# Optimization experiments

Measured on AMD Instinct MI355X. Metric: run time of the kernel, lower is better.

Reference implementation:

```python
import jax, jax.numpy as jnp
import numpy as np

B, H, W, ENC = 64, 14, 14, 2048
A, E, D, V, T = 512, 512, 512, 10000, 21


def setup_inputs() -> dict:
    key = jax.random.key(0)
    ks = jax.random.split(key, 24)
    f = lambda k, shape, s: (jax.random.normal(k, shape, jnp.float32) * s)
    inp = {
        'encoder_out': f(ks[0], (B, H, W, ENC), 1.0),
        'encoded_captions': jax.random.randint(ks[1], (B, T), 0, V),
        'caption_lengths': jax.random.randint(ks[2], (B,), 0, T + 1),
        'emb': jax.random.uniform(ks[3], (V, E), jnp.float32, -0.1, 0.1),
        'enc_att_W': f(ks[4], (ENC, A), 0.02), 'enc_att_b': jnp.zeros((A,), jnp.float32),
        'dec_att_W': f(ks[5], (D, A), 0.04), 'dec_att_b': jnp.zeros((A,), jnp.float32),
        'full_att_W': f(ks[6], (A, 1), 0.04), 'full_att_b': jnp.zeros((1,), jnp.float32),
        'init_h_W': f(ks[7], (ENC, D), 0.02), 'init_h_b': jnp.zeros((D,), jnp.float32),
        'init_c_W': f(ks[8], (ENC, D), 0.02), 'init_c_b': jnp.zeros((D,), jnp.float32),
        'f_beta_W': f(ks[9], (D, ENC), 0.04), 'f_beta_b': jnp.zeros((ENC,), jnp.float32),
        'W_ih': f(ks[10], (4 * D, E + ENC), 0.02), 'b_ih': jnp.zeros((4 * D,), jnp.float32),
        'W_hh': f(ks[11], (4 * D, D), 0.04), 'b_hh': jnp.zeros((4 * D,), jnp.float32),
        'fc_W': jax.random.uniform(ks[12], (D, V), jnp.float32, -0.1, 0.1),
        'fc_b': jnp.zeros((V,), jnp.float32),
    }
    return inp


def reference(encoder_out, encoded_captions, caption_lengths, emb,
              enc_att_W, enc_att_b, dec_att_W, dec_att_b, full_att_W, full_att_b,
              init_h_W, init_h_b, init_c_W, init_c_b, f_beta_W, f_beta_b,
              W_ih, b_ih, W_hh, b_hh, fc_W, fc_b):
    b = encoder_out.shape[0]
    enc = encoder_out.reshape(b, -1, encoder_out.shape[-1])  # (B, P, ENC)
    cl = jnp.clip(caption_lengths.reshape(-1), 1, None)
    sort_ind = jnp.argsort(-cl)  # descending by length
    cl = cl[sort_ind]
    enc = enc[sort_ind]
    caps = encoded_captions[sort_ind]
    dec_len = cl - 1  # (B,)

    embs = emb[caps]  # (B, T, E)
    mean_enc = enc.mean(axis=1)
    h0 = jnp.tanh(mean_enc @ init_h_W + init_h_b)
    c0 = jnp.tanh(mean_enc @ init_c_W + init_c_b)

    att1 = enc @ enc_att_W + enc_att_b  # (B, P, A), loop-invariant
    Tdec = caps.shape[1] - 1
    embs_t = jnp.swapaxes(embs[:, :Tdec], 0, 1)  # (Tdec, B, E)

    def step(carry, xs):
        h, c = carry
        t, x_emb = xs
        active = (t < dec_len)[:, None]  # (B,1)
        att2 = h @ dec_att_W + dec_att_b  # (B, A)
        e = jnp.squeeze(jax.nn.relu(att1 + att2[:, None, :]) @ full_att_W, -1) + full_att_b[0]  # (B,P)
        alpha = jax.nn.softmax(e + 1e-8, axis=1)
        awe = jnp.einsum('bpe,bp->be', enc, alpha)  # (B, ENC)
        gate = jax.nn.sigmoid(h @ f_beta_W + f_beta_b)
        awe = gate * awe
        x = jnp.concatenate([x_emb, awe], axis=1)  # (B, E+ENC)
        gates = x @ W_ih.T + b_ih + h @ W_hh.T + b_hh  # (B, 4D)
        i, f, g, o = jnp.split(gates, 4, axis=1)
        c_new = jax.nn.sigmoid(f) * c + jax.nn.sigmoid(i) * jnp.tanh(g)
        h_new = jax.nn.sigmoid(o) * jnp.tanh(c_new)
        preds = h_new @ fc_W + fc_b
        h = jnp.where(active, h_new, h)
        c = jnp.where(active, c_new, c)
        preds = jnp.where(active, preds, 0.0)
        alpha = jnp.where(active, alpha, 0.0)
        return (h, c), (preds, alpha)

    (_, _), (preds, alphas) = jax.lax.scan(step, (h0, c0), (jnp.arange(Tdec), embs_t))
    predictions = jnp.swapaxes(preds, 0, 1)  # (B, Tdec, V)
    alphas = jnp.swapaxes(alphas, 0, 1)      # (B, Tdec, P)
    return predictions, caps, dec_len, alphas, sort_ind
```

## Files before the change

kernel.cpp:

```cpp
#include <hip/hip_runtime.h>
#include <hip/hip_cooperative_groups.h>
#include <cstddef>


namespace cg = cooperative_groups;

namespace {

typedef _Float16 f16;
typedef f16 f16x8 __attribute__((ext_vector_type(8)));
typedef f16 f16x4 __attribute__((ext_vector_type(4)));
typedef f16 f16x2 __attribute__((ext_vector_type(2)));
typedef float f32x4 __attribute__((ext_vector_type(4)));

constexpr int NB = 64, NP = 196, NE = 2048, NA = 512, ND = 512, NV = 10000;
constexpr int NT_CAP = 21, NTD = 20;
constexpr int KC = 3072;
constexpr int LDT = 40;
constexpr int LDK = 72;

constexpr size_t OFF_ATT1   = 0;
constexpr size_t OFF_DAW    = 12845056;
constexpr size_t OFF_FBW    = 13369344;
constexpr size_t OFF_EAW    = 15466496;
constexpr size_t OFF_IHW    = 17563648;
constexpr size_t OFF_ICW    = 19660800;
constexpr size_t OFF_FCW    = 15466496;
constexpr size_t OFF_WCAT   = 25755648;
constexpr size_t OFF_MEAN16 = 38338560;
constexpr size_t OFF_H16    = 38600704;
constexpr size_t OFF_HNEW16 = 38666240;
constexpr size_t OFF_C      = 38731776;
constexpr size_t OFF_ATT2   = 38862848;
constexpr size_t OFF_GATE   = 38993920;
constexpr size_t OFF_ALPHA  = 39518208;
constexpr size_t OFF_XCAT   = 39569408;
constexpr size_t OFF_INT    = 39962624;
constexpr size_t OFF_BCAT   = 39970816;
constexpr size_t OFF_ENC16  = 39979008;
constexpr size_t FULL_BYTES = 91359232;
constexpr size_t OFF_HSEQ   = FULL_BYTES;
constexpr size_t FULL2_BYTES = FULL_BYTES + (size_t)NTD * NB * ND * 2;
constexpr size_t OFF_HWHH   = FULL2_BYTES;
constexpr size_t OFF_EMBW   = OFF_HWHH + 524288;
constexpr size_t OFF_EMBS   = OFF_EMBW + 10485760;
constexpr size_t FULL3_BYTES = OFF_EMBS + 1310720;

__device__ __forceinline__ float sigmoidf_(float x) { return 1.0f / (1.0f + expf(-x)); }

__device__ __forceinline__ void stage16(const f16* __restrict__ src, int lda, int k0,
                                        f16* __restrict__ lds, int tid) {
  const int row = tid >> 2, seg = tid & 3;
  *(f16x8*)&lds[row * LDT + seg * 8] =
      *(const f16x8*)&src[(size_t)row * lda + k0 + seg * 8];
}

__device__ __forceinline__ void cvt8(const float* __restrict__ p, f16* __restrict__ dst) {
  const float4 a = *(const float4*)p;
  const float4 b = *(const float4*)(p + 4);
  f16x8 v;
  v[0] = (f16)a.x; v[1] = (f16)a.y; v[2] = (f16)a.z; v[3] = (f16)a.w;
  v[4] = (f16)b.x; v[5] = (f16)b.y; v[6] = (f16)b.z; v[7] = (f16)b.w;
  *(f16x8*)dst = v;
}

__device__ __forceinline__ void wave_gemm64(const f16* __restrict__ A,
                                            const f16* __restrict__ Brow, int K,
                                            int kbeg, int kend,
                                            int col, int quad, f32x4* acc) {
  for (int k0 = kbeg; k0 < kend; k0 += 32) {
    const int kk = k0 + quad * 8;
    const f16x8 b = *(const f16x8*)&Brow[(size_t)col * K + kk];
#pragma unroll
    for (int mt = 0; mt < 4; ++mt) {
      const f16x8 a = *(const f16x8*)&A[(size_t)(mt * 16 + col) * K + kk];
      acc[mt] = __builtin_amdgcn_mfma_f32_16x16x32_f16(a, b, acc[mt], 0, 0, 0);
    }
  }
}

template <int MT>
__device__ __forceinline__ void wave_gemm_s(const f16* __restrict__ A, int lda,
                                            const f16* __restrict__ Brow, int ldb,
                                            int kbeg, int kend,
                                            int col, int quad, f32x4* acc) {
  for (int k0 = kbeg; k0 < kend; k0 += 32) {
    const int kk = k0 + quad * 8;
    const f16x8 b = *(const f16x8*)&Brow[(size_t)col * ldb + kk];
#pragma unroll
    for (int mt = 0; mt < MT; ++mt) {
      const f16x8 a = *(const f16x8*)&A[(size_t)(mt * 16 + col) * lda + kk];
      acc[mt] = __builtin_amdgcn_mfma_f32_16x16x32_f16(a, b, acc[mt], 0, 0, 0);
    }
  }
}

__global__ void k_sort(const int* __restrict__ cap_len, const int* __restrict__ caps,
                       int* __restrict__ perm, int* __restrict__ declen,
                       int* __restrict__ caps_sorted,
                       float* __restrict__ out_caps, float* __restrict__ out_declen,
                       float* __restrict__ out_sortind) {
  __shared__ int cl[NB];
  __shared__ int pr[NB];
  const int i = threadIdx.x;
  int c = cap_len[i];
  if (c < 1) c = 1;
  cl[i] = c;
  __syncthreads();
  int rank = 0;
  for (int j = 0; j < NB; ++j) {
    const int cj = cl[j];
    if (cj > c || (cj == c && j < i)) rank++;
  }
  pr[rank] = i;
  __syncthreads();
  const int src = pr[i];
  perm[i] = src;
  const int dl = cl[src] - 1;
  declen[i] = dl;
  out_declen[i] = (float)dl;
  out_sortind[i] = (float)src;
  for (int j = 0; j < NT_CAP; ++j) {
    const int v = caps[src * NT_CAP + j];
    caps_sorted[i * NT_CAP + j] = v;
    out_caps[i * NT_CAP + j] = (float)v;
  }
}

__global__ __launch_bounds__(256) void k_tconv(const float* __restrict__ src,
                                               f16* __restrict__ dst, int K, int Nsrc) {
  __shared__ float tile[32][33];
  const int n0 = blockIdx.x * 32, k0 = blockIdx.y * 32;
  const int tid = threadIdx.x;
  const int a = tid & 31, q = tid >> 5;
#pragma unroll
  for (int r = 0; r < 4; ++r) {
    const int kl = q * 4 + r;
    tile[a][kl] = (n0 + a < Nsrc) ? src[(size_t)(k0 + kl) * Nsrc + n0 + a] : 0.0f;
  }
  __syncthreads();
#pragma unroll
  for (int r = 0; r < 4; ++r) {
    const int nl = q * 4 + r;
    dst[(size_t)(n0 + nl) * K + k0 + a] = (f16)tile[nl][a];
  }
}

__global__ __launch_bounds__(256) void k_cvt_wcat2(const float* __restrict__ Wih,
                                                   const float* __restrict__ Whh,
                                                   const float* __restrict__ bih,
                                                   const float* __restrict__ bhh,
                                                   f16* __restrict__ Wcat2,
                                                   float* __restrict__ bcat) {
  const int r = blockIdx.x;
  const int d = r >> 2, g = r & 3;
  const int n = g * 512 + d;
  for (int k = threadIdx.x; k < KC; k += 256) {
    const float v = (k < 2560) ? Wih[(size_t)n * 2560 + k] : Whh[(size_t)n * 512 + (k - 2560)];
    Wcat2[(size_t)r * KC + k] = (f16)v;
  }
  if (threadIdx.x == 0) bcat[r] = bih[n] + bhh[n];
}

__global__ __launch_bounds__(256) void k_mean(const float* __restrict__ enc,
                                              const int* __restrict__ perm,
                                              f16* __restrict__ mean16) {
  const int b = blockIdx.y;
  const int c0 = blockIdx.x * 512 + threadIdx.x * 2;
  const float* base = enc + (size_t)perm[b] * NP * NE + c0;
  float a0 = 0.0f, a1 = 0.0f;
  for (int p = 0; p < NP; ++p) {
    const float2 v = *(const float2*)&base[(size_t)p * NE];
    a0 += v.x; a1 += v.y;
  }
  mean16[(size_t)b * NE + c0] = (f16)(a0 * (1.0f / (float)NP));
  mean16[(size_t)b * NE + c0 + 1] = (f16)(a1 * (1.0f / (float)NP));
}

__global__ __launch_bounds__(256) void k_mean16(const f16* __restrict__ enc16,
                                                f16* __restrict__ mean16) {
  const int b = blockIdx.y;
  const int c0 = blockIdx.x * 512 + threadIdx.x * 2;
  const f16* base = enc16 + (size_t)b * NP * NE + c0;
  float a0 = 0.0f, a1 = 0.0f;
  for (int p = 0; p < NP; ++p) {
    const f16x2 v = *(const f16x2*)&base[(size_t)p * NE];
    a0 += (float)v[0]; a1 += (float)v[1];
  }
  mean16[(size_t)b * NE + c0] = (f16)(a0 * (1.0f / (float)NP));
  mean16[(size_t)b * NE + c0 + 1] = (f16)(a1 * (1.0f / (float)NP));
}

__global__ __launch_bounds__(256) void k_enc_cvt(const float* __restrict__ enc,
                                                 const int* __restrict__ perm,
                                                 f16* __restrict__ enc16) {
  const int p = blockIdx.x, b = blockIdx.y;
  const float* src = enc + ((size_t)perm[b] * NP + p) * NE;
  f16* dst = enc16 + ((size_t)b * NP + p) * NE;
  const int i0 = threadIdx.x * 8;
  cvt8(src + i0, dst + i0);
}

__global__ __launch_bounds__(256) void k_embs(const float* __restrict__ emb,
                                              const int* __restrict__ caps_s,
                                              f16* __restrict__ embs16) {
  const int t = blockIdx.x, b = blockIdx.y;
  const int cap = caps_s[b * NT_CAP + t];
  const int i0 = threadIdx.x * 2;
  const float2 v = *(const float2*)(emb + (size_t)cap * 512 + i0);
  f16x2 ev; ev[0] = (f16)v.x; ev[1] = (f16)v.y;
  *(f16x2*)&embs16[((size_t)t * NB + b) * 512 + i0] = ev;
}

__global__ __launch_bounds__(256) void k_embw(const f16* __restrict__ embs16,
                                              const f16* __restrict__ Wcat2,
                                              float* __restrict__ embw) {
  __shared__ __align__(16) f16 lA[256 * LDK];
  __shared__ __align__(16) f16 lB[64 * LDK];
  const int n0 = blockIdx.x * 64, m0 = blockIdx.y * 256;
  const int tid = threadIdx.x, lane = tid & 63, wv = tid >> 6;
  const int col = lane & 15, quad = lane >> 4;
  const f16* gA = embs16 + (size_t)(m0 + tid) * 512;
  const f16* gB = Wcat2 + (size_t)(n0 + (tid >> 2)) * KC + (tid & 3) * 16;
  f16* wA = &lA[tid * LDK];
  f16* wB = &lB[(tid >> 2) * LDK + (tid & 3) * 16];
  f32x4 acc[4][4] = {};
  for (int k0 = 0; k0 < 512; k0 += 64) {
// ... 40 lines not shown
                                                   const float* __restrict__ icb,
                                                   f16* __restrict__ h16,
                                                   float* __restrict__ cst) {
  const int which = blockIdx.y;
  const f16* Wt = which ? icWt : ihWt;
  const float* bias = which ? icb : ihb;
  const int tid = threadIdx.x, lane = tid & 63, wv = tid >> 6;
  const int col = lane & 15, quad = lane >> 4;
  const int nt = blockIdx.x * 4 + wv;
  f32x4 acc[4] = {};
  wave_gemm64(mean16, Wt + (size_t)nt * 16 * NE, NE, 0, NE, col, quad, acc);
  const int n = nt * 16 + col;
#pragma unroll
  for (int mt = 0; mt < 4; ++mt) {
#pragma unroll
    for (int rr = 0; rr < 4; ++rr) {
      const int m = mt * 16 + quad * 4 + rr;
      const float v = tanhf(acc[mt][rr] + bias[n]);
      if (which == 0) h16[(size_t)m * ND + n] = (f16)v;
      else            cst[(size_t)m * ND + n] = v;
    }
  }
}

template <bool E16>
__global__ __launch_bounds__(256) void k_att1_mfma(const float* __restrict__ encf,
                                                   const f16* __restrict__ enc16,
                                                   const int* __restrict__ perm,
                                                   const f16* __restrict__ eaWt,
                                                   const float* __restrict__ eab,
                                                   f16* __restrict__ att1) {
  __shared__ __align__(16) f16 lA[64 * LDT];
  __shared__ __align__(16) f16 lB[128 * LDT];
  __shared__ int rowoff[64];
  const int r0 = blockIdx.y * 64;
  const int n0 = blockIdx.x * 128;
  const int tid = threadIdx.x, lane = tid & 63, wv = tid >> 6;
  const int col = lane & 15, quad = lane >> 4;
  if (!E16) {
    if (tid < 64) {
      const int r = r0 + tid;
      const int b = r / NP, p = r - b * NP;
      rowoff[tid] = (perm[b] * NP + p) * NE;
    }
    __syncthreads();
  }
  f32x4 acc[8] = {};
  for (int k0 = 0; k0 < NE; k0 += 32) {
    if (E16) {
      stage16(enc16 + (size_t)r0 * NE, NE, k0, lA, tid);
    } else {
      const int row = tid >> 2, seg = tid & 3;
      cvt8(encf + (size_t)rowoff[row] + k0 + seg * 8, &lA[row * LDT + seg * 8]);
    }
    {
      const int row0 = tid >> 2, seg = tid & 3;
#pragma unroll
      for (int u = 0; u < 2; ++u) {
        const int row = row0 + 64 * u;
        *(f16x8*)&lB[row * LDT + seg * 8] =
            *(const f16x8*)&eaWt[(size_t)(n0 + row) * NE + k0 + seg * 8];
      }
    }
    __syncthreads();
    const f16x8 a = *(const f16x8*)&lA[(wv * 16 + col) * LDT + quad * 8];
#pragma unroll
    for (int ns = 0; ns < 8; ++ns) {
      const f16x8 b = *(const f16x8*)&lB[(ns * 16 + col) * LDT + quad * 8];
      acc[ns] = __builtin_amdgcn_mfma_f32_16x16x32_f16(a, b, acc[ns], 0, 0, 0);
    }
    __syncthreads();
  }
#pragma unroll
  for (int ns = 0; ns < 8; ++ns) {
    const int n = n0 + ns * 16 + col;
#pragma unroll
    for (int rr = 0; rr < 4; ++rr) {
      const int r = r0 + wv * 16 + quad * 4 + rr;
      att1[(size_t)r * NA + n] = (f16)(acc[ns][rr] + eab[n]);
    }
  }
}

__global__ __launch_bounds__(256) void k_att1_v2(const f16* __restrict__ enc16,
                                                 const f16* __restrict__ eaWt,
                                                 const float* __restrict__ eab,
                                                 f16* __restrict__ att1) {
  __shared__ __align__(16) f16 lA[64 * LDK];
  __shared__ __align__(16) f16 lB[128 * LDK];
  const int r0 = blockIdx.x * 64, n0 = blockIdx.y * 128;
  const int tid = threadIdx.x, lane = tid & 63, wv = tid >> 6;
  const int col = lane & 15, quad = lane >> 4;
  const int wr = wv >> 1, wc = wv & 1;
  const int arow = tid >> 2, aseg = (tid & 3) * 16;
  const int brow = tid >> 1, bseg = (tid & 1) * 32;
  const f16* gA = enc16 + (size_t)(r0 + arow) * NE + aseg;
  const f16* gB = eaWt + (size_t)(n0 + brow) * NE + bseg;
  f16* wA = &lA[arow * LDK + aseg];
  f16* wB = &lB[brow * LDK + bseg];
  f32x4 acc[2][4] = {};
  for (int k0 = 0; k0 < NE; k0 += 64) {
    *(f16x8*)(wA)      = *(const f16x8*)(gA + k0);
    *(f16x8*)(wA + 8)  = *(const f16x8*)(gA + k0 + 8);
    *(f16x8*)(wB)      = *(const f16x8*)(gB + k0);
    *(f16x8*)(wB + 8)  = *(const f16x8*)(gB + k0 + 8);
    *(f16x8*)(wB + 16) = *(const f16x8*)(gB + k0 + 16);
    *(f16x8*)(wB + 24) = *(const f16x8*)(gB + k0 + 24);
    __syncthreads();
#pragma unroll
    for (int kh = 0; kh < 2; ++kh) {
      f16x8 a[2], b[4];
#pragma unroll
      for (int i = 0; i < 2; ++i)
        a[i] = *(const f16x8*)&lA[(wr * 32 + i * 16 + col) * LDK + kh * 32 + quad * 8];
#pragma unroll
      for (int j = 0; j < 4; ++j)
        b[j] = *(const f16x8*)&lB[(wc * 64 + j * 16 + col) * LDK + kh * 32 + quad * 8];
#pragma unroll
      for (int i = 0; i < 2; ++i)
#pragma unroll
        for (int j = 0; j < 4; ++j)
          acc[i][j] = __builtin_amdgcn_mfma_f32_16x16x32_f16(a[i], b[j], acc[i][j], 0, 0, 0);
    }
    __syncthreads();
  }
#pragma unroll
  for (int j = 0; j < 4; ++j) {
    const int n = n0 + wc * 64 + j * 16 + col;
    const float bv = eab[n];
#pragma unroll
    for (int i = 0; i < 2; ++i)
#pragma unroll
      for (int rr = 0; rr < 4; ++rr) {
        const int r = r0 + wr * 32 + i * 16 + quad * 4 + rr;
        att1[(size_t)r * NA + n] = (f16)(acc[i][j][rr] + bv);
      }
  }
}

struct StepParams {
  f16* h16;
  const f16* daWt; const float* dab;
  const f16* fbWt; const float* fbb;
  const f16* Wcat2; const float* bcat;
  const f16* att1; const float* fullW;
  const f16* enc16;
  const float* embw;
  const int* declen;
  float* att2; float* gate; float* hwhh;
  float* alpha; float* out_alphas;
  f16* xcat;
  float* cst;
  f16* hseq;
};

__global__ __launch_bounds__(512, 2) void k_steps(StepParams P) {
  cg::grid_group grid = cg::this_grid();
  __shared__ float S[8192];
  const int tid = threadIdx.x, lane = tid & 63, wv = tid >> 6;
  const int col = lane & 15, quad = lane >> 4;
  const int bid = blockIdx.x, nblk = gridDim.x;

  for (int t = 0; t < NTD; ++t) {
    for (int nt = bid; nt < 288; nt += nblk) {
      const f16* Brow; int ldb;
      if (nt < 32)       { Brow = P.daWt + (size_t)nt * 16 * ND; ldb = ND; }
      else if (nt < 160) { Brow = P.fbWt + (size_t)(nt - 32) * 16 * ND; ldb = ND; }
      else               { Brow = P.Wcat2 + (size_t)(nt - 160) * 16 * KC + 2560; ldb = KC; }
      f32x4 acc[4] = {};
      wave_gemm_s<4>(P.h16, ND, Brow, ldb, wv * 64, wv * 64 + 64, col, quad, acc);
#pragma unroll
      for (int mt = 0; mt < 4; ++mt)
#pragma unroll
        for (int rr = 0; rr < 4; ++rr)
          S[wv * 1024 + (mt * 4 + rr) * 64 + lane] = acc[mt][rr];
      __syncthreads();
#pragma unroll
      for (int j = 0; j < 2; ++j) {
        const int slot = tid * 2 + j;
        float s = S[slot];
#pragma unroll
        for (int w = 1; w < 8; ++w) s += S[w * 1024 + slot];
        const int c2 = slot >> 6, lane_s = slot & 63;
        const int mt = c2 >> 2, rr = c2 & 3;
        const int m = mt * 16 + (lane_s >> 4) * 4 + rr;
        const int nl = lane_s & 15;
        if (nt < 32) {
          const int n = nt * 16 + nl;
          P.att2[(size_t)m * NA + n] = s + P.dab[n];
        } else if (nt < 160) {
          const int n = (nt - 32) * 16 + nl;
          P.gate[(size_t)m * NE + n] = sigmoidf_(s + P.fbb[n]);
        } else {
          const int r = (nt - 160) * 16 + nl;
          P.hwhh[(size_t)m * NE + r] = s;
        }
      }
      __syncthreads();
    }
    __threadfence();
    grid.sync();

    for (int b = bid; b < NB; b += nblk) {
      float a2r[8], fwr[8];
      {
        const float4* A2 = (const float4*)(P.att2 + (size_t)b * NA + lane * 8);
        const float4* FW = (const float4*)(P.fullW + lane * 8);
        const float4 q0 = A2[0], q1 = A2[1], w0 = FW[0], w1 = FW[1];
        a2r[0] = q0.x; a2r[1] = q0.y; a2r[2] = q0.z; a2r[3] = q0.w;
        a2r[4] = q1.x; a2r[5] = q1.y; a2r[6] = q1.z; a2r[7] = q1.w;
        fwr[0] = w0.x; fwr[1] = w0.y; fwr[2] = w0.z; fwr[3] = w0.w;
        fwr[4] = w1.x; fwr[5] = w1.y; fwr[6] = w1.z; fwr[7] = w1.w;
      }
      for (int p = wv; p < NP; p += 8) {
        const f16x8 row = *(const f16x8*)(P.att1 + ((size_t)b * NP + p) * NA + lane * 8);
        float acc = 0.0f;
#pragma unroll
        for (int j = 0; j < 8; ++j) acc += fmaxf((float)row[j] + a2r[j], 0.0f) * fwr[j];
#pragma unroll
        for (int off = 32; off > 0; off >>= 1) acc += __shfl_down(acc, off, 64);
        if (lane == 0) S[p] = acc;
      }
      __syncthreads();
      if (wv == 0) {
        const float v0 = S[lane];
        const float v1 = S[lane + 64];
        const float v2 = S[lane + 128];
        const float v3 = (lane < 4) ? S[192 + lane] : -INFINITY;
        float mx = fmaxf(fmaxf(v0, v1), fmaxf(v2, v3));
#pragma unroll
        for (int off = 32; off > 0; off >>= 1) mx = fmaxf(mx, __shfl_xor(mx, off, 64));
        float s = expf(v0 - mx) + expf(v1 - mx) + expf(v2 - mx) +
                  ((lane < 4) ? expf(v3 - mx) : 0.0f);
#pragma unroll
        for (int off = 32; off > 0; off >>= 1) s += __shfl_xor(s, off, 64);
        if (lane == 0) { S[200] = mx; S[201] = 1.0f / s; }
      }
      __syncthreads();
      if (tid < NP) {
        const float a = expf(S[tid] - S[200]) * S[201];
        P.alpha[(size_t)b * NP + tid] = a;
        const bool act = t < P.declen[b];
        P.out_alphas[((size_t)b * NTD + t) * NP + tid] = act ? a : 0.0f;
      }
      __syncthreads();
    }
    __threadfence();
    grid.sync();

    for (int task = bid; task < 256; task += nblk) {
      const int b = task >> 2, q = task & 3;
      if (tid < NP) S[tid] = P.alpha[(size_t)b * NP + tid];
      __syncthreads();
      const int cl = (tid & 255) * 2, ph = tid >> 8;
      const int c = q * 512 + cl;
      const f16* base = P.enc16 + (size_t)b * NP * NE + c;
      float a0 = 0.0f, a1 = 0.0f;
      const int p0 = ph ? 98 : 0, p1 = ph ? 196 : 98;
      for (int p = p0; p < p1; ++p) {
        const f16x2 v = *(const f16x2*)&base[(size_t)p * NE];
        const float ap = S[p];
        a0 += ap * (float)v[0]; a1 += ap * (float)v[1];
      }
      S[256 + ph * 512 + cl] = a0;
      S[256 + ph * 512 + cl + 1] = a1;
      __syncthreads();
      if (tid < 256) {
        const int c2 = tid * 2;
        const float r0 = S[256 + c2] + S[768 + c2];
        const float r1 = S[256 + c2 + 1] + S[768 + c2 + 1];
        const int cc = q * 512 + c2;
        const float2 g = *(const float2*)&P.gate[(size_t)b * NE + cc];
        f16x2 o; o[0] = (f16)(r0 * g.x); o[1] = (f16)(r1 * g.y);
        *(f16x2*)&P.xcat[(size_t)b * KC + 512 + cc] = o;
      }
      __syncthreads();
    }
    __threadfence();
    grid.sync();

    for (int task = bid; task < 256; task += nblk) {
      const int nt = task >> 1, mh = task & 1;
      f32x4 acc[2] = {};
      wave_gemm_s<2>(P.xcat + (size_t)mh * 32 * KC, KC,
                     P.Wcat2 + (size_t)nt * 16 * KC, KC,
                     512 + wv * 256, 512 + wv * 256 + 256, col, quad, acc);
#pragma unroll
      for (int mt = 0; mt < 2; ++mt)
#pragma unroll
        for (int rr = 0; rr < 4; ++rr)
          S[wv * 512 + (mt * 4 + rr) * 64 + lane] = acc[mt][rr];
      __syncthreads();
      {
        float s = S[tid];
#pragma unroll
        for (int w = 1; w < 8; ++w) s += S[w * 512 + tid];
        S[tid] = s;
      }
      __syncthreads();
      if (tid < 128) {
        const int ml = tid >> 2, dl = tid & 3;
        const int m = mh * 32 + ml;
        const int d = nt * 4 + dl;
        const int mt = ml >> 4, qd = (ml >> 2) & 3, rr = ml & 3;
        float g4[4];
#pragma unroll
        for (int g = 0; g < 4; ++g) {
          const int cv = dl * 4 + g;
          const int r = nt * 16 + cv;
          g4[g] = S[(mt * 4 + rr) * 64 + qd * 16 + cv] + P.bcat[r] +
                  P.hwhh[(size_t)m * NE + r] + P.embw[((size_t)t * NB + m) * NE + r];
        }
        const float iv = sigmoidf_(g4[0]);
        const float fv = sigmoidf_(g4[1]);
        const float gv = tanhf(g4[2]);
        const float ov = sigmoidf_(g4[3]);
        const float cold = P.cst[(size_t)m * ND + d];
        const float cn = fv * cold + iv * gv;
        const float hn = ov * tanhf(cn);
        P.hseq[((size_t)t * NB + m) * ND + d] = (f16)hn;
        if (t < P.declen[m]) {
          P.cst[(size_t)m * ND + d] = cn;
          P.h16[(size_t)m * ND + d] = (f16)hn;
        }
      }
      __syncthreads();
    }
    __threadfence();
    grid.sync();
  }
}

__global__ __launch_bounds__(256) void k_hgemm_v2(const f16* __restrict__ h16,
                                                  const f16* __restrict__ daWt,
                                                  const float* __restrict__ dab,
                                                  const f16* __restrict__ fbWt,
                                                  const float* __restrict__ fbb,
                                                  float* __restrict__ att2,
                                                  float* __restrict__ gate) {
  __shared__ float R[2 * 64 * 16];
  const int tid = threadIdx.x, lane = tid & 63, wv = tid >> 6;
  const int col = lane & 15, quad = lane >> 4;
  const int sub = wv >> 1, kh = wv & 1;
  const int nt = blockIdx.x * 2 + sub;
  const bool is_att = nt < 32;
  const f16* Brow = is_att ? (daWt + (size_t)nt * 16 * ND)
                           : (fbWt + (size_t)(nt - 32) * 16 * ND);
  f32x4 acc[4] = {};
  wave_gemm64(h16, Brow, ND, kh * 256, kh * 256 + 256, col, quad, acc);
  if (kh) {
#pragma unroll
    for (int mt = 0; mt < 4; ++mt)
#pragma unroll
      for (int rr = 0; rr < 4; ++rr)
        R[(sub * 64 + lane) * 16 + mt * 4 + rr] = acc[mt][rr];
  }
  __syncthreads();
  if (kh) return;
#pragma unroll
  for (int mt = 0; mt < 4; ++mt)
#pragma unroll
    for (int rr = 0; rr < 4; ++rr)
      acc[mt][rr] += R[(sub * 64 + lane) * 16 + mt * 4 + rr];
  if (is_att) {
    const int n = nt * 16 + col;
#pragma unroll
    for (int mt = 0; mt < 4; ++mt)
#pragma unroll
      for (int rr = 0; rr < 4; ++rr) {
        const int m = mt * 16 + quad * 4 + rr;
        att2[(size_t)m * NA + n] = acc[mt][rr] + dab[n];
      }
  } else {
    const int n = (nt - 32) * 16 + col;
#pragma unroll
    for (int mt = 0; mt < 4; ++mt)
#pragma unroll
      for (int rr = 0; rr < 4; ++rr) {
        const int m = mt * 16 + quad * 4 + rr;
        gate[(size_t)m * NE + n] = sigmoidf_(acc[mt][rr] + fbb[n]);
      }
  }
}

template <bool E16>
__global__ __launch_bounds__(512) void k_attn_awe(const f16* __restrict__ att1,
                                                  const float* __restrict__ att2,
                                                  const float* __restrict__ fullW,
                                                  const int* __restrict__ declen, int t,
                                                  const float* __restrict__ encf,
                                                  const f16* __restrict__ enc16,
                                                  const int* __restrict__ perm,
                                                  const float* __restrict__ gate,
                                                  const float* __restrict__ emb,
// ... 402 lines not shown
    const float cold = cst[(size_t)m * ND + d];
    const float cn = fv * cold + iv * gv;
    const float hn = ov * tanhf(cn);
    hnew16[(size_t)m * ND + d] = (f16)hn;
    hseq[((size_t)t * NB + m) * ND + d] = (f16)hn;
    if (t < declen[m]) {
      cst[(size_t)m * ND + d] = cn;
      h16[(size_t)m * ND + d] = (f16)hn;
    }
  }
}

}

extern "C" void kernel_launch(void* const* d_in, const int* in_sizes, int n_in,
                              void* d_out, int out_size, void* d_ws, size_t ws_size,
                              hipStream_t stream) {
  const float* enc        = (const float*)d_in[0];
  const int*   caps       = (const int*)d_in[1];
  const int*   caplen     = (const int*)d_in[2];
  const float* emb        = (const float*)d_in[3];
  const float* enc_att_W  = (const float*)d_in[4];
  const float* enc_att_b  = (const float*)d_in[5];
  const float* dec_att_W  = (const float*)d_in[6];
  const float* dec_att_b  = (const float*)d_in[7];
  const float* full_att_W = (const float*)d_in[8];
  const float* init_h_W   = (const float*)d_in[10];
  const float* init_h_b   = (const float*)d_in[11];
  const float* init_c_W   = (const float*)d_in[12];
  const float* init_c_b   = (const float*)d_in[13];
  const float* f_beta_W   = (const float*)d_in[14];
  const float* f_beta_b   = (const float*)d_in[15];
  const float* W_ih       = (const float*)d_in[16];
  const float* b_ih       = (const float*)d_in[17];
  const float* W_hh       = (const float*)d_in[18];
  const float* b_hh       = (const float*)d_in[19];
  const float* fc_W       = (const float*)d_in[20];
  const float* fc_b       = (const float*)d_in[21];

  char* ws = (char*)d_ws;
  f16*   att1   = (f16*)(ws + OFF_ATT1);
  f16*   daWt   = (f16*)(ws + OFF_DAW);
  f16*   fbWt   = (f16*)(ws + OFF_FBW);
  f16*   eaWt   = (f16*)(ws + OFF_EAW);
  f16*   ihWt   = (f16*)(ws + OFF_IHW);
  f16*   icWt   = (f16*)(ws + OFF_ICW);
  f16*   fcWt   = (f16*)(ws + OFF_FCW);
  f16*   Wcat2  = (f16*)(ws + OFF_WCAT);
  f16*   mean16 = (f16*)(ws + OFF_MEAN16);
  f16*   h16    = (f16*)(ws + OFF_H16);
  f16*   hnew16 = (f16*)(ws + OFF_HNEW16);
  float* cst    = (float*)(ws + OFF_C);
  float* att2   = (float*)(ws + OFF_ATT2);
  float* gate   = (float*)(ws + OFF_GATE);
  float* alpha  = (float*)(ws + OFF_ALPHA);
  f16*   xcat   = (f16*)(ws + OFF_XCAT);
  int*   wsi    = (int*)(ws + OFF_INT);
  int*   perm   = wsi;
  int*   declen = wsi + 64;
  int*   caps_s = wsi + 128;
  float* bcat   = (float*)(ws + OFF_BCAT);
  f16*   enc16  = (f16*)(ws + OFF_ENC16);
  float* hwhh   = (float*)(ws + OFF_HWHH);
  float* embw   = (float*)(ws + OFF_EMBW);
  f16*   embs16 = (f16*)(ws + OFF_EMBS);

  const bool full  = ws_size >= FULL_BYTES;
  const bool batch = ws_size >= FULL2_BYTES;
  const bool full3 = ws_size >= FULL3_BYTES;
  f16* hseq = batch ? (f16*)(ws + OFF_HSEQ) : (f16*)nullptr;

  bool coop_ok = false;
  int coop_grid = 0;
  if (full3) {
    int dev = 0;
    if (hipGetDevice(&dev) == hipSuccess) {
      int coop = 0;
      hipDeviceGetAttribute(&coop, hipDeviceAttributeCooperativeLaunch, dev);
      if (coop) {
        int ncu = 0;
        hipDeviceGetAttribute(&ncu, hipDeviceAttributeMultiprocessorCount, dev);
        int maxb = 0;
        if (hipOccupancyMaxActiveBlocksPerMultiprocessor(
                &maxb, reinterpret_cast<const void*>(&k_steps), 512, 0) == hipSuccess &&
            maxb >= 1 && ncu > 0) {
          coop_grid = maxb * ncu;
          if (coop_grid > 256) coop_grid = 256;
          coop_ok = coop_grid >= 64;
        }
      }
    }
  }

  float* out         = (float*)d_out;
  float* out_pred    = out;
  float* out_caps    = out_pred + (size_t)NB * NTD * NV;
  float* out_declen  = out_caps + (size_t)NB * NT_CAP;
  float* out_alphas  = out_declen + NB;
  float* out_sortind = out_alphas + (size_t)NB * NTD * NP;

  k_sort<<<1, 64, 0, stream>>>(caplen, caps, perm, declen, caps_s,
                               out_caps, out_declen, out_sortind);
  k_tconv<<<dim3(16, 64), 256, 0, stream>>>(enc_att_W, eaWt, 2048, 512);
  k_tconv<<<dim3(16, 16), 256, 0, stream>>>(dec_att_W, daWt, 512, 512);
  k_tconv<<<dim3(64, 16), 256, 0, stream>>>(f_beta_W, fbWt, 512, 2048);
  k_tconv<<<dim3(16, 64), 256, 0, stream>>>(init_h_W, ihWt, 2048, 512);
  k_tconv<<<dim3(16, 64), 256, 0, stream>>>(init_c_W, icWt, 2048, 512);
  if (full) {
    k_enc_cvt<<<dim3(196, 64), 256, 0, stream>>>(enc, perm, enc16);
    k_mean16<<<dim3(4, 64), 256, 0, stream>>>(enc16, mean16);
  } else {
    k_mean<<<dim3(4, 64), 256, 0, stream>>>(enc, perm, mean16);
  }
  k_init_mfma<<<dim3(16, 2), 256, 0, stream>>>(mean16, ihWt, icWt, init_h_b, init_c_b,
                                               h16, cst);
  if (full)
    k_att1_v2<<<dim3(196, 4), 256, 0, stream>>>(enc16, eaWt, enc_att_b, att1);
  else
    k_att1_mfma<false><<<dim3(4, 196), 256, 0, stream>>>(enc, enc16, perm, eaWt,
                                                         enc_att_b, att1);
  k_tconv<<<dim3(314, 16), 256, 0, stream>>>(fc_W, fcWt, 512, NV);
  k_cvt_wcat2<<<2048, 256, 0, stream>>>(W_ih, W_hh, b_ih, b_hh, Wcat2, bcat);
  if (full3) {
    k_embs<<<dim3(NTD, NB), 256, 0, stream>>>(emb, caps_s, embs16);
    k_embw<<<dim3(32, 5), 256, 0, stream>>>(embs16, Wcat2, embw);
  }

  if (full3 && coop_ok) {
    StepParams P;
    P.h16 = h16; P.daWt = daWt; P.dab = dec_att_b; P.fbWt = fbWt; P.fbb = f_beta_b;
    P.Wcat2 = Wcat2; P.bcat = bcat; P.att1 = att1; P.fullW = full_att_W;
    P.enc16 = enc16; P.embw = embw; P.declen = declen;
    P.att2 = att2; P.gate = gate; P.hwhh = hwhh; P.alpha = alpha;
    P.out_alphas = out_alphas; P.xcat = xcat; P.cst = cst; P.hseq = hseq;
    void* args[] = { &P };
    hipLaunchCooperativeKernel(reinterpret_cast<const void*>(&k_steps),
                               dim3(coop_grid), dim3(512), args, 0, stream);
    k_fc_v2<<<dim3(157, 5), 256, 0, stream>>>(hseq, fcWt, fc_b, declen, out_pred);
  } else if (full3) {
    for (int t = 0; t < NTD; ++t) {
      k_hall<<<288, 256, 0, stream>>>(h16, daWt, dec_att_b, fbWt, f_beta_b, Wcat2,
                                      att2, gate, hwhh);
      k_logits<<<NB, 512, 0, stream>>>(att1, att2, full_att_W, declen, t,
                                       alpha, out_alphas);
      k_awe<<<256, 256, 0, stream>>>(enc16, alpha, gate, xcat);
      k_xlstm_v3<<<256, 512, 0, stream>>>(xcat, Wcat2, bcat, hwhh, embw, declen, t,
                                          cst, h16, hnew16, hseq);
    }
    k_fc_v2<<<dim3(157, 5), 256, 0, stream>>>(hseq, fcWt, fc_b, declen, out_pred);
  } else {
    for (int t = 0; t < NTD; ++t) {
      k_hgemm_v2<<<80, 256, 0, stream>>>(h16, daWt, dec_att_b, fbWt, f_beta_b,
                                         att2, gate);
      if (full)
        k_attn_awe<true><<<NB, 512, 0, stream>>>(att1, att2, full_att_W, declen, t,
                                                 enc, enc16, perm, gate, emb, caps_s,
                                                 h16, xcat, out_alphas);
      else
        k_attn_awe<false><<<NB, 512, 0, stream>>>(att1, att2, full_att_W, declen, t,
                                                  enc, enc16, perm, gate, emb, caps_s,
                                                  h16, xcat, out_alphas);
      k_xlstm_v2<<<128, 512, 0, stream>>>(xcat, Wcat2, bcat, declen, t,
                                          cst, h16, hnew16, hseq);
      if (!batch)
        k_fc_mfma<<<157, 256, 0, stream>>>(hnew16, fcWt, fc_b, declen, t, out_pred);
    }
    if (batch)
      k_fc_v2<<<dim3(157, 5), 256, 0, stream>>>(hseq, fcWt, fc_b, declen, out_pred);
  }
}
```

Measured before the change: 1.305 ms.

## Fuse per-step attention phases into one per-batch task, removing two grid syncs

The cooperative step kernel now computes att2, the attention softmax, the weighted encoding and the f_beta gate inside a single per-(batch, quarter) task, using dot products against an LDS copy of h. This removes two grid-wide barriers and the global att2/gate/alpha/hwhh buffers per step. The h·W_hh term moves into the LSTM GEMM by widening its K range to include the copied h in xcat. In exchange, att2 and the softmax are recomputed redundantly four times per batch row, and the GEMVs run on scalar dot2 instead of MFMA. Separately, the weight-transpose launches are merged and the att1 GEMM tile grows to 128x128.

Measured after the change: 5.115 ms. +291.9%, slower.

```diff
diff --git a/kernel.cpp b/kernel.cpp
--- a/kernel.cpp
+++ b/kernel.cpp
@@ -48,6 +48,25 @@
 
 __device__ __forceinline__ float sigmoidf_(float x) { return 1.0f / (1.0f + expf(-x)); }
 
+__device__ __forceinline__ float dot8_(const f16* __restrict__ a,
+                                       const f16* __restrict__ b, float s) {
+  const f16x8 av = *(const f16x8*)a;
+  const f16x8 bv = *(const f16x8*)b;
+#if __has_builtin(__builtin_amdgcn_fdot2)
+#pragma unroll
+  for (int j = 0; j < 4; ++j) {
+    f16x2 a2, b2;
+    a2[0] = av[j * 2]; a2[1] = av[j * 2 + 1];
+    b2[0] = bv[j * 2]; b2[1] = bv[j * 2 + 1];
+    s = __builtin_amdgcn_fdot2(a2, b2, s, false);
+  }
+#else
+#pragma unroll
+  for (int j = 0; j < 8; ++j) s += (float)av[j] * (float)bv[j];
+#endif
+  return s;
+}
+
 __device__ __forceinline__ void stage16(const f16* __restrict__ src, int lda, int k0,
                                         f16* __restrict__ lds, int tid) {
   const int row = tid >> 2, seg = tid & 3;
@@ -143,6 +162,51 @@
   for (int r = 0; r < 4; ++r) {
     const int nl = q * 4 + r;
     dst[(size_t)(n0 + nl) * K + k0 + a] = (f16)tile[nl][a];
+  }
+}
+
+__global__ __launch_bounds__(256) void k_tconv3(const float* __restrict__ s0, f16* d0,
+                                                const float* __restrict__ s1, f16* d1,
+                                                const float* __restrict__ s2, f16* d2) {
+  __shared__ float tile[32][33];
+  const float* src = (blockIdx.z == 0) ? s0 : (blockIdx.z == 1) ? s1 : s2;
+  f16* dst = (blockIdx.z == 0) ? d0 : (blockIdx.z == 1) ? d1 : d2;
+  const int n0 = blockIdx.x * 32, k0 = blockIdx.y * 32;
+  const int tid = threadIdx.x;
+  const int a = tid & 31, q = tid >> 5;
+#pragma unroll
+  for (int r = 0; r < 4; ++r) {
+    const int kl = q * 4 + r;
+    tile[a][kl] = src[(size_t)(k0 + kl) * 512 + n0 + a];
+  }
+  __syncthreads();
+#pragma unroll
+  for (int r = 0; r < 4; ++r) {
+    const int nl = q * 4 + r;
+    dst[(size_t)(n0 + nl) * 2048 + k0 + a] = (f16)tile[nl][a];
+  }
+}
+
+__global__ __launch_bounds__(256) void k_tconv2b(const float* __restrict__ sd, f16* dd,
+                                                 const float* __restrict__ sf, f16* df) {
+  __shared__ float tile[32][33];
+  const bool is_d = blockIdx.x < 16;
+  const float* src = is_d ? sd : sf;
+  f16* dst = is_d ? dd : df;
+  const int nsrc = is_d ? 512 : 2048;
+  const int n0 = (is_d ? blockIdx.x : (blockIdx.x - 16)) * 32, k0 = blockIdx.y * 32;
+  const int tid = threadIdx.x;
+  const int a = tid & 31, q = tid >> 5;
+#pragma unroll
+  for (int r = 0; r < 4; ++r) {
+    const int kl = q * 4 + r;
+    tile[a][kl] = src[(size_t)(k0 + kl) * nsrc + n0 + a];
+  }
+  __syncthreads();
+#pragma unroll
+  for (int r = 0; r < 4; ++r) {
+    const int nl = q * 4 + r;
+    dst[(size_t)(n0 + nl) * 512 + k0 + a] = (f16)tile[nl][a];
   }
 }
 
@@ -349,42 +413,40 @@
   }
 }
 
-__global__ __launch_bounds__(256) void k_att1_v2(const f16* __restrict__ enc16,
+__global__ __launch_bounds__(256) void k_att1_v3(const f16* __restrict__ enc16,
                                                  const f16* __restrict__ eaWt,
                                                  const float* __restrict__ eab,
                                                  f16* __restrict__ att1) {
-  __shared__ __align__(16) f16 lA[64 * LDK];
+  __shared__ __align__(16) f16 lA[128 * LDK];
   __shared__ __align__(16) f16 lB[128 * LDK];
-  const int r0 = blockIdx.x * 64, n0 = blockIdx.y * 128;
+  const int r0 = blockIdx.x * 128, n0 = blockIdx.y * 128;
   const int tid = threadIdx.x, lane = tid & 63, wv = tid >> 6;
   const int col = lane & 15, quad = lane >> 4;
   const int wr = wv >> 1, wc = wv & 1;
-  const int arow = tid >> 2, aseg = (tid & 3) * 16;
-  const int brow = tid >> 1, bseg = (tid & 1) * 32;
-  const f16* gA = enc16 + (size_t)(r0 + arow) * NE + aseg;
-  const f16* gB = eaWt + (size_t)(n0 + brow) * NE + bseg;
-  f16* wA = &lA[arow * LDK + aseg];
-  f16* wB = &lB[brow * LDK + bseg];
-  f32x4 acc[2][4] = {};
+  const int srow = tid >> 1, sseg = (tid & 1) * 32;
+  const f16* gA = enc16 + (size_t)(r0 + srow) * NE + sseg;
+  const f16* gB = eaWt + (size_t)(n0 + srow) * NE + sseg;
+  f16* wA = &lA[srow * LDK + sseg];
+  f16* wB = &lB[srow * LDK + sseg];
+  f32x4 acc[4][4] = {};
   for (int k0 = 0; k0 < NE; k0 += 64) {
-    *(f16x8*)(wA)      = *(const f16x8*)(gA + k0);
-    *(f16x8*)(wA + 8)  = *(const f16x8*)(gA + k0 + 8);
-    *(f16x8*)(wB)      = *(const f16x8*)(gB + k0);
-    *(f16x8*)(wB + 8)  = *(const f16x8*)(gB + k0 + 8);
-    *(f16x8*)(wB + 16) = *(const f16x8*)(gB + k0 + 16);
-    *(f16x8*)(wB + 24) = *(const f16x8*)(gB + k0 + 24);
+#pragma unroll
+    for (int u = 0; u < 4; ++u) {
+      *(f16x8*)(wA + u * 8) = *(const f16x8*)(gA + k0 + u * 8);
+      *(f16x8*)(wB + u * 8) = *(const f16x8*)(gB + k0 + u * 8);
+    }
     __syncthreads();
 #pragma unroll
     for (int kh = 0; kh < 2; ++kh) {
-      f16x8 a[2], b[4];
-#pragma unroll
-      for (int i = 0; i < 2; ++i)
-        a[i] = *(const f16x8*)&lA[(wr * 32 + i * 16 + col) * LDK + kh * 32 + quad * 8];
+      f16x8 a[4], b[4];
+#pragma unroll
+      for (int i = 0; i < 4; ++i)
+        a[i] = *(const f16x8*)&lA[(wr * 64 + i * 16 + col) * LDK + kh * 32 + quad * 8];
 #pragma unroll
       for (int j = 0; j < 4; ++j)
         b[j] = *(const f16x8*)&lB[(wc * 64 + j * 16 + col) * LDK + kh * 32 + quad * 8];
 #pragma unroll
-      for (int i = 0; i < 2; ++i)
+      for (int i = 0; i < 4; ++i)
 #pragma unroll
         for (int j = 0; j < 4; ++j)
           acc[i][j] = __builtin_amdgcn_mfma_f32_16x16x32_f16(a[i], b[j], acc[i][j], 0, 0, 0);
@@ -396,16 +458,16 @@
     const int n = n0 + wc * 64 + j * 16 + col;
     const float bv = eab[n];
 #pragma unroll
-    for (int i = 0; i < 2; ++i)
+    for (int i = 0; i < 4; ++i)
 #pragma unroll
       for (int rr = 0; rr < 4; ++rr) {
-        const int r = r0 + wr * 32 + i * 16 + quad * 4 + rr;
+        const int r = r0 + wr * 64 + i * 16 + quad * 4 + rr;
         att1[(size_t)r * NA + n] = (f16)(acc[i][j][rr] + bv);
       }
   }
 }
 
-struct StepParams {
+struct Step2Params {
   f16* h16;
   const f16* daWt; const float* dab;
   const f16* fbWt; const float* fbb;
@@ -414,86 +476,63 @@
   const f16* enc16;
   const float* embw;
   const int* declen;
-  float* att2; float* gate; float* hwhh;
-  float* alpha; float* out_alphas;
+  float* out_alphas;
   f16* xcat;
   float* cst;
   f16* hseq;
 };
 
-__global__ __launch_bounds__(512, 2) void k_steps(StepParams P) {
+__global__ __launch_bounds__(512, 2) void k_steps2(Step2Params P) {
   cg::grid_group grid = cg::this_grid();
-  __shared__ float S[8192];
+  __shared__ float S[4096];
+  float* att2L = S;
+  float* eL    = S + 512;
+  float* alL   = S + 712;
+  float* redL  = S + 912;
+  f16*   hL    = (f16*)(S + 1024);
+  float* partL = S + 1280;
   const int tid = threadIdx.x, lane = tid & 63, wv = tid >> 6;
   const int col = lane & 15, quad = lane >> 4;
   const int bid = blockIdx.x, nblk = gridDim.x;
 
   for (int t = 0; t < NTD; ++t) {
-    for (int nt = bid; nt < 288; nt += nblk) {
-      const f16* Brow; int ldb;
-      if (nt < 32)       { Brow = P.daWt + (size_t)nt * 16 * ND; ldb = ND; }
-      else if (nt < 160) { Brow = P.fbWt + (size_t)(nt - 32) * 16 * ND; ldb = ND; }
-      else               { Brow = P.Wcat2 + (size_t)(nt - 160) * 16 * KC + 2560; ldb = KC; }
-      f32x4 acc[4] = {};
-      wave_gemm_s<4>(P.h16, ND, Brow, ldb, wv * 64, wv * 64 + 64, col, quad, acc);
-#pragma unroll
-      for (int mt = 0; mt < 4; ++mt)
-#pragma unroll
-        for (int rr = 0; rr < 4; ++rr)
-          S[wv * 1024 + (mt * 4 + rr) * 64 + lane] = acc[mt][rr];
+    for (int task = bid; task < 256; task += nblk) {
+      const int b = task >> 2, q = task & 3;
+      if (tid < 64)
+        ((f16x8*)hL)[tid] = ((const f16x8*)(P.h16 + (size_t)b * ND))[tid];
       __syncthreads();
-#pragma unroll
-      for (int j = 0; j < 2; ++j) {
-        const int slot = tid * 2 + j;
-        float s = S[slot];
-#pragma unroll
-        for (int w = 1; w < 8; ++w) s += S[w * 1024 + slot];
-        const int c2 = slot >> 6, lane_s = slot & 63;
-        const int mt = c2 >> 2, rr = c2 & 3;
-        const int m = mt * 16 + (lane_s >> 4) * 4 + rr;
-        const int nl = lane_s & 15;
-        if (nt < 32) {
-          const int n = nt * 16 + nl;
-          P.att2[(size_t)m * NA + n] = s + P.dab[n];
-        } else if (nt < 160) {
-          const int n = (nt - 32) * 16 + nl;
-          P.gate[(size_t)m * NE + n] = sigmoidf_(s + P.fbb[n]);
-        } else {
-          const int r = (nt - 160) * 16 + nl;
-          P.hwhh[(size_t)m * NE + r] = s;
-        }
+      {
+        const f16* wrow = P.daWt + (size_t)tid * ND;
+        float s = 0.0f;
+        for (int k = 0; k < ND; k += 8) s = dot8_(&hL[k], &wrow[k], s);
+        att2L[tid] = s + P.dab[tid];
       }
       __syncthreads();
-    }
-    __threadfence();
-    grid.sync();
-
-    for (int b = bid; b < NB; b += nblk) {
-      float a2r[8], fwr[8];
       {
-        const float4* A2 = (const float4*)(P.att2 + (size_t)b * NA + lane * 8);
+        float a2r[8], fwr[8];
+#pragma unroll
+        for (int j = 0; j < 8; ++j) a2r[j] = att2L[lane * 8 + j];
         const float4* FW = (const float4*)(P.fullW + lane * 8);
-        const float4 q0 = A2[0], q1 = A2[1], w0 = FW[0], w1 = FW[1];
-        a2r[0] = q0.x; a2r[1] = q0.y; a2r[2] = q0.z; a2r[3] = q0.w;
-        a2r[4] = q1.x; a2r[5] = q1.y; a2r[6] = q1.z; a2r[7] = q1.w;
+        const float4 w0 = FW[0], w1 = FW[1];
         fwr[0] = w0.x; fwr[1] = w0.y; fwr[2] = w0.z; fwr[3] = w0.w;
         fwr[4] = w1.x; fwr[5] = w1.y; fwr[6] = w1.z; fwr[7] = w1.w;
-      }
-      for (int p = wv; p < NP; p += 8) {
-        const f16x8 row = *(const f16x8*)(P.att1 + ((size_t)b * NP + p) * NA + lane * 8);
-        float acc = 0.0f;
-#pragma unroll
-        for (int j = 0; j < 8; ++j) acc += fmaxf((float)row[j] + a2r[j], 0.0f) * fwr[j];
-#pragma unroll
-        for (int off = 32; off > 0; off >>= 1) acc += __shfl_down(acc, off, 64);
-        if (lane == 0) S[p] = acc;
+        for (int p = wv; p < NP; p += 8) {
+          const f16x8 row = *(const f16x8*)(P.att1 + ((size_t)b * NP + p) * NA + lane * 8);
+          float acc = 0.0f;
+#pragma unroll
+          for (int j = 0; j < 8; ++j)
+            acc += fmaxf((float)row[j] + a2r[j], 0.0f) * fwr[j];
+#pragma unroll
+          for (int off = 32; off > 0; off >>= 1) acc += __shfl_down(acc, off, 64);
+          if (lane == 0) eL[p] = acc;
+        }
       }
       __syncthreads();
       if (wv == 0) {
-        const float v0 = S[lane];
-        const float v1 = S[lane + 64];
-        const float v2 = S[lane + 128];
-        const float v3 = (lane < 4) ? S[192 + lane] : -INFINITY;
+        const float v0 = eL[lane];
+        const float v1 = eL[lane + 64];
+        const float v2 = eL[lane + 128];
+        const float v3 = (lane < 4) ? eL[192 + lane] : -INFINITY;
         float mx = fmaxf(fmaxf(v0, v1), fmaxf(v2, v3));
 #pragma unroll
         for (int off = 32; off > 0; off >>= 1) mx = fmaxf(mx, __shfl_xor(mx, off, 64));
@@ -501,45 +540,52 @@
                   ((lane < 4) ? expf(v3 - mx) : 0.0f);
 #pragma unroll
         for (int off = 32; off > 0; off >>= 1) s += __shfl_xor(s, off, 64);
-        if (lane == 0) { S[200] = mx; S[201] = 1.0f / s; }
+        if (lane == 0) { redL[0] = mx; redL[1] = 1.0f / s; }
       }
       __syncthreads();
       if (tid < NP) {
-        const float a = expf(S[tid] - S[200]) * S[201];
-        P.alpha[(size_t)b * NP + tid] = a;
-        const bool act = t < P.declen[b];
-        P.out_alphas[((size_t)b * NTD + t) * NP + tid] = act ? a : 0.0f;
+        const float a = expf(eL[tid] - redL[0]) * redL[1];
+        alL[tid] = a;
+        if (q == 0) {
+          const bool act = t < P.declen[b];
+          P.out_alphas[((size_t)b * NTD + t) * NP + tid] = act ? a : 0.0f;
+        }
       }
       __syncthreads();
-    }
-    __threadfence();
-    grid.sync();
-
-    for (int task = bid; task < 256; task += nblk) {
-      const int b = task >> 2, q = task & 3;
-      if (tid < NP) S[tid] = P.alpha[(size_t)b * NP + tid];
-      __syncthreads();
-      const int cl = (tid & 255) * 2, ph = tid >> 8;
-      const int c = q * 512 + cl;
-      const f16* base = P.enc16 + (size_t)b * NP * NE + c;
-      float a0 = 0.0f, a1 = 0.0f;
-      const int p0 = ph ? 98 : 0, p1 = ph ? 196 : 98;
-      for (int p = p0; p < p1; ++p) {
-        const f16x2 v = *(const f16x2*)&base[(size_t)p * NE];
-        const float ap = S[p];
-        a0 += ap * (float)v[0]; a1 += ap * (float)v[1];
-      }
-      S[256 + ph * 512 + cl] = a0;
-      S[256 + ph * 512 + cl + 1] = a1;
+      {
+        const int cl = (tid & 255) * 2, ph = tid >> 8;
+        const int c = q * 512 + cl;
+        const f16* base = P.enc16 + (size_t)b * NP * NE + c;
+        float a0 = 0.0f, a1 = 0.0f;
+        const int p0 = ph ? 98 : 0, p1 = ph ? 196 : 98;
+        for (int p = p0; p < p1; ++p) {
+          const f16x2 v = *(const f16x2*)&base[(size_t)p * NE];
+          const float ap = alL[p];
+          a0 += ap * (float)v[0]; a1 += ap * (float)v[1];
+        }
+        partL[ph * 512 + cl] = a0;
+        partL[ph * 512 + cl + 1] = a1;
+      }
       __syncthreads();
       if (tid < 256) {
         const int c2 = tid * 2;
-        const float r0 = S[256 + c2] + S[768 + c2];
-        const float r1 = S[256 + c2 + 1] + S[768 + c2 + 1];
-        const int cc = q * 512 + c2;
-        const float2 g = *(const float2*)&P.gate[(size_t)b * NE + cc];
-        f16x2 o; o[0] = (f16)(r0 * g.x); o[1] = (f16)(r1 * g.y);
-        *(f16x2*)&P.xcat[(size_t)b * KC + 512 + cc] = o;
+        const float r0 = partL[c2] + partL[512 + c2];
+        const float r1 = partL[c2 + 1] + partL[512 + c2 + 1];
+        const int n = q * 512 + c2;
+        const f16* w0 = P.fbWt + (size_t)n * ND;
+        const f16* w1 = w0 + ND;
+        float g0 = 0.0f, g1 = 0.0f;
+        for (int k = 0; k < ND; k += 8) {
+          g0 = dot8_(&hL[k], &w0[k], g0);
+          g1 = dot8_(&hL[k], &w1[k], g1);
+        }
+        g0 = sigmoidf_(g0 + P.fbb[n]);
+        g1 = sigmoidf_(g1 + P.fbb[n + 1]);
+        f16x2 o; o[0] = (f16)(r0 * g0); o[1] = (f16)(r1 * g1);
+        *(f16x2*)&P.xcat[(size_t)b * KC + 512 + n] = o;
+      } else if (q == 0) {
+        const int i0 = (tid - 256) * 2;
+        *(f16x2*)&P.xcat[(size_t)b * KC + 2560 + i0] = *(const f16x2*)&hL[i0];
       }
       __syncthreads();
     }
@@ -551,7 +597,7 @@
       f32x4 acc[2] = {};
       wave_gemm_s<2>(P.xcat + (size_t)mh * 32 * KC, KC,
                      P.Wcat2 + (size_t)nt * 16 * KC, KC,
-                     512 + wv * 256, 512 + wv * 256 + 256, col, quad, acc);
+                     512 + wv * 320, 512 + wv * 320 + 320, col, quad, acc);
 #pragma unroll
       for (int mt = 0; mt < 2; ++mt)
 #pragma unroll
@@ -576,7 +622,7 @@
           const int cv = dl * 4 + g;
           const int r = nt * 16 + cv;
           g4[g] = S[(mt * 4 + rr) * 64 + qd * 16 + cv] + P.bcat[r] +
-                  P.hwhh[(size_t)m * NE + r] + P.embw[((size_t)t * NB + m) * NE + r];
+                  P.embw[((size_t)t * NB + m) * NE + r];
         }
         const float iv = sigmoidf_(g4[0]);
         const float fv = sigmoidf_(g4[1]);
@@ -1145,7 +1191,7 @@
         hipDeviceGetAttribute(&ncu, hipDeviceAttributeMultiprocessorCount, dev);
         int maxb = 0;
         if (hipOccupancyMaxActiveBlocksPerMultiprocessor(
-                &maxb, reinterpret_cast<const void*>(&k_steps), 512, 0) == hipSuccess &&
+                &maxb, reinterpret_cast<const void*>(&k_steps2), 512, 0) == hipSuccess &&
             maxb >= 1 && ncu > 0) {
           coop_grid = maxb * ncu;
           if (coop_grid > 256) coop_grid = 256;
@@ -1164,11 +1210,9 @@
 
   k_sort<<<1, 64, 0, stream>>>(caplen, caps, perm, declen, caps_s,
                                out_caps, out_declen, out_sortind);
-  k_tconv<<<dim3(16, 64), 256, 0, stream>>>(enc_att_W, eaWt, 2048, 512);
-  k_tconv<<<dim3(16, 16), 256, 0, stream>>>(dec_att_W, daWt, 512, 512);
-  k_tconv<<<dim3(64, 16), 256, 0, stream>>>(f_beta_W, fbWt, 512, 2048);
-  k_tconv<<<dim3(16, 64), 256, 0, stream>>>(init_h_W, ihWt, 2048, 512);
-  k_tconv<<<dim3(16, 64), 256, 0, stream>>>(init_c_W, icWt, 2048, 512);
+  k_tconv3<<<dim3(16, 64, 3), 256, 0, stream>>>(enc_att_W, eaWt, init_h_W, ihWt,
+                                                init_c_W, icWt);
+  k_tconv2b<<<dim3(80, 16), 256, 0, stream>>>(dec_att_W, daWt, f_beta_W, fbWt);
   if (full) {
     k_enc_cvt<<<dim3(196, 64), 256, 0, stream>>>(enc, perm, enc16);
     k_mean16<<<dim3(4, 64), 256, 0, stream>>>(enc16, mean16);
@@ -1178,7 +1222,7 @@
   k_init_mfma<<<dim3(16, 2), 256, 0, stream>>>(mean16, ihWt, icWt, init_h_b, init_c_b,
                                                h16, cst);
   if (full)
-    k_att1_v2<<<dim3(196, 4), 256, 0, stream>>>(enc16, eaWt, enc_att_b, att1);
+    k_att1_v3<<<dim3(98, 4), 256, 0, stream>>>(enc16, eaWt, enc_att_b, att1);
   else
     k_att1_mfma<false><<<dim3(4, 196), 256, 0, stream>>>(enc, enc16, perm, eaWt,
                                                          enc_att_b, att1);
@@ -1190,14 +1234,13 @@
   }
 
   if (full3 && coop_ok) {
-    StepParams P;
+    Step2Params P;
     P.h16 = h16; P.daWt = daWt; P.dab = dec_att_b; P.fbWt = fbWt; P.fbb = f_beta_b;
     P.Wcat2 = Wcat2; P.bcat = bcat; P.att1 = att1; P.fullW = full_att_W;
     P.enc16 = enc16; P.embw = embw; P.declen = declen;
-    P.att2 = att2; P.gate = gate; P.hwhh = hwhh; P.alpha = alpha;
     P.out_alphas = out_alphas; P.xcat = xcat; P.cst = cst; P.hseq = hseq;
     void* args[] = { &P };
-    hipLaunchCooperativeKernel(reinterpret_cast<const void*>(&k_steps),
+    hipLaunchCooperativeKernel(reinterpret_cast<const void*>(&k_steps2),
                                dim3(coop_grid), dim3(512), args, 0, stream);
     k_fc_v2<<<dim3(157, 5), 256, 0, stream>>>(hseq, fcWt, fc_b, declen, out_pred);
   } else if (full3) {
```
